# Kernel optimization log

Measured on AMD Instinct MI355X. Metric: run time of the kernel, lower is better.

The kernel has to match this reference:

```python
import jax, jax.numpy as jnp
import numpy as np

NUM_HOPS = 2
GAMMA = 0.8


def setup_inputs() -> dict:
    key = jax.random.key(0)
    ks = jax.random.split(key, 17)
    B, L, V, E, M, Mt, R = 8, 128, 50257, 768, 400, 800, 40
    W = 0.02  # init scale for learned params
    return {
        'hidden_states': jax.random.normal(ks[0], (B, L, E), jnp.float32),
        'wte': jax.random.normal(ks[1], (V, E), jnp.float32) * W,
        'rel_emb': jax.random.normal(ks[2], (R, E), jnp.float32) * W,
        'W_s': jax.random.normal(ks[3], (NUM_HOPS, E, E), jnp.float32) * W,
        'W_n': jax.random.normal(ks[4], (NUM_HOPS, E, E), jnp.float32) * W,
        'W_r': jax.random.normal(ks[5], (NUM_HOPS, E, E), jnp.float32) * W,
        'W_triple': jax.random.normal(ks[6], (E, 3 * E), jnp.float32) * W,
        'gate_w': jax.random.normal(ks[7], (E,), jnp.float32) * W,
        'gate_b': jnp.zeros((), jnp.float32),
        'concept_ids': jax.random.randint(ks[8], (B, M), 0, V),
        'relation_ids': jax.random.randint(ks[9], (B, Mt), 0, R),
        'head_idx': jax.random.randint(ks[10], (B, Mt), 0, M),
        'tail_idx': jax.random.randint(ks[11], (B, Mt), 0, M),
        'triple_labels': jax.random.randint(ks[12], (B, Mt), 0, 2),
        'distances': jax.random.randint(ks[13], (B, M), 0, 3),
        'vocab_map': jax.random.randint(ks[14], (V,), 0, M),
        'map_mask': jax.random.randint(ks[15], (V,), 0, 2),
    }


def _triple_encoder(wte, rel_emb, W_s, W_n, W_r, concept_ids, relation_ids, head_idx, tail_idx):
    concept_repr = wte[concept_ids]      # B,M,E
    rel_repr = rel_emb[relation_ids]     # B,Mt,E

    def gcn(cr, rr, h, t):               # per-batch CompGCN, faithful to torch loop
        M = cr.shape[0]
        ch, rh = cr, rr
        for l in range(NUM_HOPS):
            upd = jnp.zeros_like(cr)
            upd = upd.at[t].add(cr[h] - rr)   # scatter_add(o) + scatter_add(-rel)
            upd = upd.at[h].add(cr[t] - rr)
            cnt = jnp.zeros((M,), cr.dtype).at[t].add(1.0).at[h].add(1.0)
            upd = cr @ W_s[l].T + (upd @ W_n[l].T) / jnp.clip(cnt, 1.0, None)[:, None]
            ch = jax.nn.relu(upd)
            rh = rr @ W_r[l].T
        return ch, rh

    node, relh = jax.vmap(gcn)(concept_repr, rel_repr, head_idx, tail_idx)
    E = node.shape[-1]
    hi = jnp.broadcast_to(head_idx[:, :, None], head_idx.shape + (E,))
    ti = jnp.broadcast_to(tail_idx[:, :, None], tail_idx.shape + (E,))
    hrep = jnp.take_along_axis(node, hi, axis=1)
    trep = jnp.take_along_axis(node, ti, axis=1)
    return jnp.concatenate([hrep, relh, trep], axis=-1)  # B,Mt,3E


def _multi_hop(triple_prob, distances, head, tail):
    B, L, Mt = triple_prob.shape
    M = distances.shape[1]
    dt = triple_prob.dtype
    init_mask = jnp.broadcast_to((distances == 0).astype(dt)[:, None, :], (B, L, M))
    decay = (0.8 ** distances.astype(dt))[:, None, :]
    head_b = jnp.broadcast_to(head[:, None, :], (B, L, Mt))

    def scatter_mean(vals, t):  # vals: L,Mt  t: Mt -> L,M
        s = jnp.zeros((L, M), vals.dtype).at[:, t].add(vals)
        c = jnp.zeros((M,), vals.dtype).at[t].add(1.0)
        return s / jnp.clip(c, 1.0, None)

    node_score = init_mask
    total = init_mask * (-100000.0)
    for _ in range(NUM_HOPS):
        ths = jnp.take_along_axis(node_score, head_b, axis=2)  # B,L,Mt
        upd = ths * GAMMA + triple_prob
        node_score = jax.vmap(scatter_mean)(upd, tail)          # B,L,M
        total = total + node_score * decay
    return total


def reference(hidden_states, wte, rel_emb, W_s, W_n, W_r, W_triple, gate_w, gate_b,
              concept_ids, relation_ids, head_idx, tail_idx, triple_labels,
              distances, vocab_map, map_mask):
    triple_repr = _triple_encoder(wte, rel_emb, W_s, W_n, W_r,
                                  concept_ids, relation_ids, head_idx, tail_idx)
    lm_probs = jax.nn.softmax(hidden_states @ wte.T, axis=-1)            # B,L,V
    tl = triple_repr @ W_triple.T                                        # B,Mt,E
    triple_prob = jax.nn.sigmoid(jnp.einsum('ble,bme->blm', hidden_states, tl))
    triple_prob = triple_prob * (triple_labels != -1)[:, None, :].astype(triple_prob.dtype)
    scores = _multi_hop(triple_prob, distances, head_idx, tail_idx)      # B,L,M
    concept_probs = jax.nn.softmax(scores, axis=-1)
    cpv = concept_probs[:, :, vocab_map]                                 # gather into vocab: B,L,V
    cpv = cpv * (map_mask != 0)[None, None, :].astype(cpv.dtype)
    gate = jax.nn.sigmoid(hidden_states @ gate_w + gate_b)[..., None]    # B,L,1
    probs = gate * cpv + (1.0 - gate) * lm_probs
    return probs
```

## Files before the change

kernel.cpp:

```cpp
#include <hip/hip_runtime.h>
#include <stdint.h>

#define HB 8
#define HL 128
#define HV 50257
#define HE 768
#define HM 400
#define HMT 800
#define HBL (HB*HL)
#define NTILES 393
#define ELD 50272

typedef __attribute__((ext_vector_type(4))) float f32x4;
typedef __attribute__((ext_vector_type(8))) short bf16x8;
typedef unsigned short u16;

struct u16x4 { u16 x, y, z, w; };

__device__ __forceinline__ u16 f2bf(float x){
  union { float f; uint32_t u; } v; v.f = x;
  uint32_t r = v.u + 0x7fffu + ((v.u >> 16) & 1u);
  return (u16)(r >> 16);
}
__device__ __forceinline__ float bf2f(u16 b){
  union { uint32_t u; float f; } v; v.u = ((uint32_t)b) << 16;
  return v.f;
}
__device__ __forceinline__ void glds(const u16* g, const u16* l){
  __builtin_amdgcn_global_load_lds(
      (const __attribute__((address_space(1))) void*)g,
      (__attribute__((address_space(3))) void*)l, 16, 0, 0);
}

__global__ __launch_bounds__(256) void prep_k(const float* __restrict__ hs,
    const float* __restrict__ rel, const float* __restrict__ Wr1src,
    const float* __restrict__ Wtsrc, const float* __restrict__ Ws1,
    const float* __restrict__ Wn1, const int* __restrict__ vmap,
    const int* __restrict__ mmask, const float* __restrict__ wte,
    u16* __restrict__ hid_b, u16* __restrict__ rel_b,
    u16* __restrict__ wr1, u16* __restrict__ wt_b, u16* __restrict__ wcat,
    int* __restrict__ vmm, u16* __restrict__ wte_b){
  const int b = blockIdx.x, t = threadIdx.x;
  if (b >= 5456) {
    long i = (long)(b-5456)*256 + t;
    if (i < (long)HV*HE/4) {
      float4 x = ((const float4*)wte)[i];
      u16x4 y; y.x=f2bf(x.x); y.y=f2bf(x.y); y.z=f2bf(x.z); y.w=f2bf(x.w);
      ((u16x4*)wte_b)[i] = y;
    }
    return;
  }
  if (b < 768) {
    int i = b*256 + t;
    float4 x = ((const float4*)hs)[i];
    u16x4 y; y.x=f2bf(x.x); y.y=f2bf(x.y); y.z=f2bf(x.z); y.w=f2bf(x.w);
    ((u16x4*)hid_b)[i] = y;
  } else if (b < 798) {
    int i = (b-768)*256 + t;
    float4 x = ((const float4*)rel)[i];
    u16x4 y; y.x=f2bf(x.x); y.y=f2bf(x.y); y.z=f2bf(x.z); y.w=f2bf(x.w);
    ((u16x4*)rel_b)[i] = y;
  } else if (b < 1374) {
    int i = (b-798)*256 + t;
    float4 x = ((const float4*)Wr1src)[i];
    u16x4 y; y.x=f2bf(x.x); y.y=f2bf(x.y); y.z=f2bf(x.z); y.w=f2bf(x.w);
    ((u16x4*)wr1)[i] = y;
  } else if (b < 3102) {
    int i = (b-1374)*256 + t;
    float4 x = ((const float4*)Wtsrc)[i];
    u16x4 y; y.x=f2bf(x.x); y.y=f2bf(x.y); y.z=f2bf(x.z); y.w=f2bf(x.w);
    ((u16x4*)wt_b)[i] = y;
  } else if (b < 5406) {
    int i = (b-3102)*256 + t;
    int e = i / HE, k = i - e*HE;
    wcat[(long)e*(2*HE) + k]      = f2bf(Ws1[i]);
    wcat[(long)e*(2*HE) + HE + k] = f2bf(Wn1[i]);
  } else {
    int base = (b-5406)*1024 + t*4;
    #pragma unroll
    for (int i = 0; i < 4; ++i) {
      int c = base + i;
      if (c < HV) vmm[c] = mmask[c] ? vmap[c] : -1;
    }
  }
}

__global__ __launch_bounds__(256) void gcn_scatter_k(const float* __restrict__ wte,
    const float* __restrict__ rel, const int* __restrict__ cids,
    const int* __restrict__ rids, const int* __restrict__ head,
    const int* __restrict__ tail, u16* __restrict__ An){
  const int ch = blockIdx.x % 48;
  const int b  = blockIdx.x / 48;
  const int e0 = ch * 16;
  __shared__ float cw[HM][17];
  __shared__ float upd[HM][17];
  __shared__ float relc[40][17];
  __shared__ float cnt[HM];
  const int tid = threadIdx.x;

  for (int idx = tid; idx < HM*16; idx += 256) {
    int m = idx >> 4, e = idx & 15;
    cw[m][e] = wte[(long)cids[b*HM+m]*HE + e0 + e];
    upd[m][e] = 0.f;
  }
  for (int idx = tid; idx < 40*16; idx += 256) {
    int r = idx >> 4, e = idx & 15;
    relc[r][e] = rel[r*HE + e0 + e];
  }
  for (int m = tid; m < HM; m += 256) cnt[m] = 0.f;
  __syncthreads();

  for (int j = tid; j < HMT; j += 256) {
    int h = head[b*HMT+j], t = tail[b*HMT+j], r = rids[b*HMT+j];
    atomicAdd(&cnt[t], 1.f);
    atomicAdd(&cnt[h], 1.f);
    #pragma unroll
    for (int e = 0; e < 16; ++e) {
      float rv = relc[r][e];
      atomicAdd(&upd[t][e], cw[h][e] - rv);
      atomicAdd(&upd[h][e], cw[t][e] - rv);
    }
  }
  __syncthreads();

  for (int idx = tid; idx < HM*16; idx += 256) {
    int m = idx >> 4, e = idx & 15;
    float ic = 1.f / fmaxf(cnt[m], 1.f);
    u16* dst = An + ((long)b*HM + m) * (2*HE);
    dst[e0 + e]      = f2bf(cw[m][e]);
    dst[HE + e0 + e] = f2bf(upd[m][e] * ic);
  }
}

template<int ACT, int OUTBF16, int BIG, int DBUF>
__device__ __forceinline__ void gemm_core(
    const u16* __restrict__ Ab, const u16* __restrict__ Bb,
    void* __restrict__ Cout, float* __restrict__ rowpart,
    int Mdim, int Ndim, int Kdim, int lda, int ldb, int ldc,
    int mtile, int ntile, u16* AsmB, u16* BsmB)
{
  const int m0 = mtile * 128;
  const int n0 = ntile * 128;
  const int tid = threadIdx.x;
  const int lane = tid & 63;
  const int wid = tid >> 6;
  const int wr = wid >> 1, wc = wid & 1;
  const int srw = lane >> 3;
  const int sl  = lane & 7;

  f32x4 acc[4][4] = {};

  auto stage = [&](int buf, int k0) {
    u16* As = AsmB + buf*8192;
    u16* Bs = BsmB + buf*8192;
    #pragma unroll
    for (int i = 0; i < 4; ++i) {
      const int c = i*4 + wid;
      const int row = c*8 + srw;
      const int koff = k0 + ((sl ^ srw) * 8);
      int ra = m0 + row; if (ra > Mdim-1) ra = Mdim-1;
      glds(Ab + (long)ra * lda + koff, &As[c*512]);
      int rn = n0 + row; if (rn > Ndim-1) rn = Ndim-1;
      glds(Bb + (long)rn * ldb + koff, &Bs[c*512]);
    }
  };
  auto compute = [&](int buf) {
    const u16* As = AsmB + buf*8192;
    const u16* Bs = BsmB + buf*8192;
    #pragma unroll
    for (int kk = 0; kk < 2; ++kk) {
      bf16x8 af[4], bfr[4];
      #pragma unroll
      for (int mi = 0; mi < 4; ++mi) {
        const int R = wr*64 + mi*16 + (lane & 15);
        af[mi] = *(const bf16x8*)&As[R*64 + (((kk*4 + (lane>>4)) ^ (R & 7)) * 8)];
      }
      #pragma unroll
      for (int ni = 0; ni < 4; ++ni) {
        const int R = wc*64 + ni*16 + (lane & 15);
        bfr[ni] = *(const bf16x8*)&Bs[R*64 + (((kk*4 + (lane>>4)) ^ (R & 7)) * 8)];
      }
      #pragma unroll
      for (int mi = 0; mi < 4; ++mi)
        #pragma unroll
        for (int ni = 0; ni < 4; ++ni)
          acc[mi][ni] = __builtin_amdgcn_mfma_f32_16x16x32_bf16(af[mi], bfr[ni], acc[mi][ni], 0, 0, 0);
    }
  };

  const int NT = Kdim >> 6;
  if (DBUF) {
    stage(0, 0);
    __syncthreads();
    int cur = 0;
    for (int t = 0; t < NT; ++t) {
      if (t + 1 < NT) stage(cur ^ 1, (t + 1) << 6);
      compute(cur);
      __syncthreads();
      cur ^= 1;
    }
  } else {
    for (int t = 0; t < NT; ++t) {
      stage(0, t << 6);
      __syncthreads();
      compute(0);
      __syncthreads();
    }
  }

  const int cr0 = m0 + wr*64 + ((lane >> 4) * 4);
  const int cc0 = n0 + wc*64 + (lane & 15);

  if (BIG) {
    float* rs = (float*)AsmB;
    #pragma unroll
    for (int mi = 0; mi < 4; ++mi) {
      #pragma unroll
      for (int r = 0; r < 4; ++r) {
        const int rowi = cr0 + mi*16 + r;
        float s = 0.f;
        #pragma unroll
        for (int ni = 0; ni < 4; ++ni) {
          const int col = cc0 + ni*16;
          if (col < Ndim) {
            float e = __expf(acc[mi][ni][r]);
            if (OUTBF16) ((u16*)Cout)[(long)rowi*ELD + col] = f2bf(e);
            else        ((float*)Cout)[(long)rowi*HV + col] = e;
            s += e;
          }
        }
        s += __shfl_xor(s, 8); s += __shfl_xor(s, 4);
        s += __shfl_xor(s, 2); s += __shfl_xor(s, 1);
        if ((lane & 15) == 0)
          rs[wc*128 + wr*64 + mi*16 + ((lane >> 4) << 2) + r] = s;
      }
    }
    __syncthreads();
    if (tid < 128)
      rowpart[(long)(m0 + tid) * NTILES + ntile] = rs[tid] + rs[128 + tid];
    return;
  }

  #pragma unroll
  for (int mi = 0; mi < 4; ++mi) {
    #pragma unroll
    for (int ni = 0; ni < 4; ++ni) {
      const int col = cc0 + ni*16;
      if (col < Ndim) {
        #pragma unroll
        for (int r = 0; r < 4; ++r) {
          const int rowi = cr0 + mi*16 + r;
          if (rowi < Mdim) {
            float v = acc[mi][ni][r];
            if (ACT == 1) v = fmaxf(v, 0.f);
            if (OUTBF16) ((u16*)Cout)[(long)rowi*ldc + col] = f2bf(v);
            else        ((float*)Cout)[(long)rowi*ldc + col] = v;
          }
        }
      }
    }
  }
}

template<int ACT, int OUTBF16, int BIG>
__global__ __launch_bounds__(256) void gemm_bt(
    const u16* __restrict__ A, const u16* __restrict__ Bm,
    void* __restrict__ Cout, float* __restrict__ rowpart,
    int Mdim, int Ndim, int Kdim, int lda, int ldb, int ldc,
    long Abs, long Bbs, long Cbs)
{
  __shared__ alignas(16) u16 Asm[(BIG ? 1 : 2)*8192];
  __shared__ alignas(16) u16 Bsm[(BIG ? 1 : 2)*8192];
  int mtile, ntile, bz;
  if (BIG) {
    const int wg = (blockIdx.x & 7) * NTILES + (blockIdx.x >> 3);
    mtile = wg & 7; ntile = wg >> 3; bz = 0;
  } else {
    mtile = blockIdx.x; ntile = blockIdx.y; bz = blockIdx.z;
  }
  const u16* Ab = A + (long)bz * Abs;
  const u16* Bb = Bm + (long)bz * Bbs;
  void* Cb = OUTBF16 ? (void*)((u16*)Cout + (long)bz * Cbs)
                     : (void*)((float*)Cout + (long)bz * Cbs);
  gemm_core<ACT,OUTBF16,BIG,(BIG?0:1)>(Ab, Bb, Cb, rowpart, Mdim, Ndim, Kdim,
                                       lda, ldb, ldc, mtile, ntile, Asm, Bsm);
}

template<int PHASE>
__global__ __launch_bounds__(256) void gemm_multi(
    const u16* __restrict__ anode, const u16* __restrict__ wcat,
    u16* __restrict__ nodeb, const u16* __restrict__ rel_b,
    const u16* __restrict__ wr1, u16* __restrict__ relWr,
    const u16* __restrict__ wt_b, u16* __restrict__ P13)
{
  __shared__ alignas(16) u16 Asm[2*8192];
  __shared__ alignas(16) u16 Bsm[2*8192];
  const int mtile = blockIdx.x, ntile = blockIdx.y, z = blockIdx.z;
  if (PHASE == 0) {
    if (z < 8) {
      gemm_core<1,1,0,1>(anode + (long)z*HM*2*HE, wcat, nodeb + (long)z*HM*HE,
          nullptr, HM, HE, 2*HE, 2*HE, 2*HE, HE, mtile, ntile, Asm, Bsm);
    } else {
      if (mtile) return;
      gemm_core<0,1,0,1>(rel_b, wr1, relWr, nullptr,
          40, HE, HE, HE, HE, HE, 0, ntile, Asm, Bsm);
    }
  } else {
    if (z < 8) {
      if (mtile) return;
      gemm_core<0,1,0,1>(relWr, wt_b + HE, P13 + (long)z*840*HE + (long)800*HE,
          nullptr, 40, HE, HE, HE, 3*HE, HE, 0, ntile, Asm, Bsm);
    } else if (z < 16) {
      gemm_core<0,1,0,1>(nodeb + (long)(z-8)*HM*HE, wt_b,
          P13 + (long)(z-8)*840*HE, nullptr,
          HM, HE, HE, HE, 3*HE, HE, mtile, ntile, Asm, Bsm);
    } else {
      gemm_core<0,1,0,1>(nodeb + (long)(z-16)*HM*HE, wt_b + 2*HE,
          P13 + (long)(z-16)*840*HE + (long)HM*HE, nullptr,
          HM, HE, HE, HE, 3*HE, HE, mtile, ntile, Asm, Bsm);
    }
  }
}

__global__ __launch_bounds__(256) void multihop_k(const float* __restrict__ scores,
    const float* __restrict__ hs, const float* __restrict__ gw,
    const float* __restrict__ gb,
    const int* __restrict__ head, const int* __restrict__ tail,
    const int* __restrict__ rids, const int* __restrict__ labels,
    const int* __restrict__ dist, float* __restrict__ gatev,
    float* __restrict__ cprob){
  const int bl = blockIdx.x;
  const int b = bl >> 7;
  const int tid = threadIdx.x;
  const int lane = tid & 63, wid = tid >> 6;
  __shared__ float srow[840];
  __shared__ float tp[HMT];
  __shared__ float ns[HM], sacc[HM], tot[HM], invc[HM], dec[HM];
  __shared__ float red[16];
  __shared__ float gred[4];
  const int* hb = head + b*HMT;
  const int* tb = tail + b*HMT;
  const int* rb = rids + b*HMT;
  const int* lb = labels + b*HMT;
  const float* sr = scores + (long)bl * 840;

  float gs = 0.f;
  for (int e = tid; e < HE; e += 256) gs += hs[(long)bl*HE + e] * gw[e];
  for (int o = 32; o; o >>= 1) gs += __shfl_down(gs, o);
  if (lane == 0) gred[wid] = gs;

  for (int i = tid; i < 840; i += 256) srow[i] = sr[i];
  for (int m = tid; m < HM; m += 256) {
    int d = dist[b*HM + m];
    float im = (d == 0) ? 1.f : 0.f;
    ns[m] = im; tot[m] = im * -100000.f;
    dec[m] = (d == 0) ? 1.f : ((d == 1) ? 0.8f : 0.64f);
    sacc[m] = 0.f; invc[m] = 0.f;
  }
  __syncthreads();
  if (tid == 0)
    gatev[bl] = 1.f / (1.f + __expf(-(gred[0]+gred[1]+gred[2]+gred[3] + gb[0])));
  for (int j = tid; j < HMT; j += 256) {
    atomicAdd(&invc[tb[j]], 1.f);
    float x = srow[hb[j]] + srow[400 + tb[j]] + srow[800 + rb[j]];
    tp[j] = (lb[j] == -1) ? 0.f : 1.f / (1.f + __expf(-x));
  }
  __syncthreads();
  for (int m = tid; m < HM; m += 256) invc[m] = 1.f / fmaxf(invc[m], 1.f);
  __syncthreads();

  for (int hop = 0; hop < 2; ++hop) {
    for (int j = tid; j < HMT; j += 256) {
      float u = ns[hb[j]] * 0.8f + tp[j];
      atomicAdd(&sacc[tb[j]], u);
    }
    __syncthreads();
    for (int m = tid; m < HM; m += 256) {
      float v = sacc[m] * invc[m];
      ns[m] = v; tot[m] += v * dec[m]; sacc[m] = 0.f;
    }
    __syncthreads();
  }

  float lmx = -3.4e38f;
  for (int m = tid; m < HM; m += 256) lmx = fmaxf(lmx, tot[m]);
  for (int o = 32; o; o >>= 1) lmx = fmaxf(lmx, __shfl_down(lmx, o));
  if (lane == 0) red[wid] = lmx;
  __syncthreads();
  float gmx = fmaxf(fmaxf(red[0], red[1]), fmaxf(red[2], red[3]));
  float ls = 0.f;
  for (int m = tid; m < HM; m += 256) ls += __expf(tot[m] - gmx);
  for (int o = 32; o; o >>= 1) ls += __shfl_down(ls, o);
  if (lane == 0) red[8 + wid] = ls;
  __syncthreads();
  float inv = 1.f / (red[8] + red[9] + red[10] + red[11]);
  float* outrow = cprob + (long)bl * HM;
  for (int m = tid; m < HM; m += 256) outrow[m] = __expf(tot[m] - gmx) * inv;
}

template<int EXPBF>
__global__ __launch_bounds__(256) void finalize_k(const void* __restrict__ expl,
    const float* __restrict__ rowpart, const float* __restrict__ gatev,
    const float* __restrict__ cprob, const int* __restrict__ vmm,
    float* __restrict__ out){
  const int r = blockIdx.x / 13;
  const int ch = blockIdx.x - r*13;
  const int tid = threadIdx.x;
  __shared__ float red[4];
  __shared__ float cpl[HM];
  float s = 0.f;
  for (int t = tid; t < NTILES; t += 256) s += rowpart[r*NTILES + t];
  for (int o = 32; o; o >>= 1) s += __shfl_down(s, o);
  if ((tid & 63) == 0) red[tid >> 6] = s;
  const float g = gatev[r];
  for (int m = tid; m < HM; m += 256) cpl[m] = g * cprob[r*HM + m];
  __syncthreads();
  const float scale = (1.f - g) / (red[0] + red[1] + red[2] + red[3]);
  const u16* erb = (const u16*)expl + (long)r * ELD;
  const float* erf = (const float*)expl + (long)r * HV;
  float* orow = out + (long)r * HV;
  #pragma unroll
  for (int it = 0; it < 2; ++it) {
    const int c = ch*4096 + it*2048 + tid*8;
    if (c + 8 <= HV) {
      float e[8];
      if (EXPBF) {
        bf16x8 v = *(const bf16x8*)&erb[c];
        #pragma unroll
        for (int i = 0; i < 8; ++i) e[i] = bf2f((u16)v[i]);
      } else {
        float4 a = *(const float4*)&erf[c];
        float4 b2 = *(const float4*)&erf[c+4];
        e[0]=a.x; e[1]=a.y; e[2]=a.z; e[3]=a.w;
        e[4]=b2.x; e[5]=b2.y; e[6]=b2.z; e[7]=b2.w;
      }
      int4 v0 = *(const int4*)&vmm[c];
      int4 v1 = *(const int4*)&vmm[c+4];
      const int ix[8] = {v0.x, v0.y, v0.z, v0.w, v1.x, v1.y, v1.z, v1.w};
      float o8[8];
      #pragma unroll
      for (int i = 0; i < 8; ++i)
        o8[i] = (ix[i] >= 0 ? cpl[ix[i]] : 0.f) + scale * e[i];
      *(float4*)&orow[c]   = make_float4(o8[0], o8[1], o8[2], o8[3]);
      *(float4*)&orow[c+4] = make_float4(o8[4], o8[5], o8[6], o8[7]);
    } else if (c < HV) {
      for (int i = 0; i < 8 && c + i < HV; ++i) {
        float e = EXPBF ? bf2f(((const u16*)expl)[(long)r*ELD + c + i]) : erf[c+i];
        int ix = vmm[c+i];
        orow[c+i] = (ix >= 0 ? cpl[ix] : 0.f) + scale * e;
      }
    }
  }
}

extern "C" void kernel_launch(void* const* d_in, const int* in_sizes, int n_in,
                              void* d_out, int out_size, void* d_ws, size_t ws_size,
                              hipStream_t stream)
{
  const float* hs   = (const float*)d_in[0];
  const float* wte  = (const float*)d_in[1];
  const float* rel  = (const float*)d_in[2];
  const float* Ws   = (const float*)d_in[3];
  const float* Wn   = (const float*)d_in[4];
  const float* Wr   = (const float*)d_in[5];
  const float* Wt   = (const float*)d_in[6];
  const float* gw   = (const float*)d_in[7];
  const float* gb   = (const float*)d_in[8];
  const int* cids   = (const int*)d_in[9];
  const int* rids   = (const int*)d_in[10];
  const int* head   = (const int*)d_in[11];
  const int* tail   = (const int*)d_in[12];
  const int* labels = (const int*)d_in[13];
  const int* dist   = (const int*)d_in[14];
  const int* vmap   = (const int*)d_in[15];
  const int* mmask  = (const int*)d_in[16];
  float* out = (float*)d_out;

  char* ws = (char*)d_ws;
  size_t o = 0;
  auto alloc = [&](size_t bytes) -> char* {
    char* p = ws + o; o = (o + bytes + 255) & ~(size_t)255; return p;
  };
  u16* wte_b     = (u16*)alloc((size_t)HV*HE*2);
  u16* hid_b     = (u16*)alloc((size_t)HBL*HE*2);
  float* cprob   = (float*)alloc((size_t)HBL*HM*4);
  float* rowpart = (float*)alloc((size_t)HBL*NTILES*4);
  float* gatev   = (float*)alloc(HBL*4);
  int* vmm       = (int*)alloc((size_t)HV*4);

  const bool bigws = ws_size >= (size_t)196*1024*1024;
  u16* expl = (u16*)(ws + o);
  u16* wcat  = (u16*)alloc((size_t)HE*2*HE*2);
  u16* wr1   = (u16*)alloc((size_t)HE*HE*2);
  u16* wt_b  = (u16*)alloc((size_t)HE*3*HE*2);
  u16* rel_b = (u16*)alloc((size_t)40*HE*2);
  u16* anode = (u16*)alloc((size_t)HB*HM*2*HE*2);
  u16* nodeb = (u16*)alloc((size_t)HB*HM*HE*2);
  u16* relWr = (u16*)alloc((size_t)40*HE*2);
  float* scores = (float*)alloc((size_t)HB*HL*840*4);
  u16* P13   = (u16*)alloc((size_t)HB*840*HE*2);
  (void)in_sizes; (void)n_in; (void)out_size;

  prep_k<<<5456 + 37693, 256, 0, stream>>>(hs, rel, Wr + (size_t)HE*HE, Wt,
      Ws + (size_t)HE*HE, Wn + (size_t)HE*HE, vmap, mmask, wte,
      hid_b, rel_b, wr1, wt_b, wcat, vmm, wte_b);

  gcn_scatter_k<<<HB*48, 256, 0, stream>>>(wte, rel, cids, rids, head, tail, anode);

  gemm_multi<0><<<dim3(4,6,9), 256, 0, stream>>>(anode, wcat, nodeb,
      rel_b, wr1, relWr, wt_b, P13);
  gemm_multi<1><<<dim3(4,6,24), 256, 0, stream>>>(anode, wcat, nodeb,
      rel_b, wr1, relWr, wt_b, P13);
  gemm_bt<0,0,0><<<dim3(1,7,8), 256, 0, stream>>>(hid_b, P13, scores,
      nullptr, HL, 840, HE, HE, HE, 840, (long)HL*HE, (long)840*HE, (long)HL*840);

  multihop_k<<<HBL, 256, 0, stream>>>(scores, hs, gw, gb, head, tail, rids,
      labels, dist, gatev, cprob);

  if (bigws) {
    gemm_bt<0,1,1><<<3144, 256, 0, stream>>>(hid_b, wte_b, expl, rowpart,
        HBL, HV, HE, HE, HE, ELD, 0, 0, 0);
    finalize_k<1><<<HBL*13, 256, 0, stream>>>(expl, rowpart, gatev, cprob,
        vmm, out);
  } else {
    gemm_bt<0,0,1><<<3144, 256, 0, stream>>>(hid_b, wte_b, out, rowpart,
        HBL, HV, HE, HE, HE, HV, 0, 0, 0);
    finalize_k<0><<<HBL*13, 256, 0, stream>>>(out, rowpart, gatev, cprob,
        vmm, out);
  }
}
```

Measured before the change: 449.2 us.

## Reassociate triple scoring through hidden·W_triple and fuse multihop into vocab GEMM

The triple-score path is reassociated: instead of projecting node and relation representations through W_triple and then multiplying by hidden states, hidden states are first multiplied by a transposed W_triple (hw = hid·Wt), and then scored against node and relation embeddings. This removes the per-batch P13 intermediate and merges the small GEMMs into two flat-grid launches. The multihop softmax kernel is folded into the large vocab GEMM launch as extra blocks sharing a union of shared memory, which cuts launches and lets that work overlap with the GEMM. The cost is a strided, uncoalesced transpose of W_triple in prep and larger shared memory per block for the fused kernel.

```diff
diff --git a/kernel.cpp b/kernel.cpp
--- a/kernel.cpp
+++ b/kernel.cpp
@@ -34,11 +34,11 @@
 
 __global__ __launch_bounds__(256) void prep_k(const float* __restrict__ hs,
     const float* __restrict__ rel, const float* __restrict__ Wr1src,
-    const float* __restrict__ Wtsrc, const float* __restrict__ Ws1,
+    const float* __restrict__ Wt, const float* __restrict__ Ws1,
     const float* __restrict__ Wn1, const int* __restrict__ vmap,
     const int* __restrict__ mmask, const float* __restrict__ wte,
     u16* __restrict__ hid_b, u16* __restrict__ rel_b,
-    u16* __restrict__ wr1, u16* __restrict__ wt_b, u16* __restrict__ wcat,
+    u16* __restrict__ wr1, u16* __restrict__ wtT, u16* __restrict__ wcat,
     int* __restrict__ vmm, u16* __restrict__ wte_b){
   const int b = blockIdx.x, t = threadIdx.x;
   if (b >= 5456) {
@@ -66,10 +66,14 @@
     u16x4 y; y.x=f2bf(x.x); y.y=f2bf(x.y); y.z=f2bf(x.z); y.w=f2bf(x.w);
     ((u16x4*)wr1)[i] = y;
   } else if (b < 3102) {
-    int i = (b-1374)*256 + t;
-    float4 x = ((const float4*)Wtsrc)[i];
-    u16x4 y; y.x=f2bf(x.x); y.y=f2bf(x.y); y.z=f2bf(x.z); y.w=f2bf(x.w);
-    ((u16x4*)wt_b)[i] = y;
+    int g = (b-1374)*256 + t;
+    int f = g / 192, r = g - f*192, e0 = r*4;
+    u16x4 y;
+    y.x = f2bf(Wt[(long)(e0+0)*2304 + f]);
+    y.y = f2bf(Wt[(long)(e0+1)*2304 + f]);
+    y.z = f2bf(Wt[(long)(e0+2)*2304 + f]);
+    y.w = f2bf(Wt[(long)(e0+3)*2304 + f]);
+    *(u16x4*)&wtT[(long)f*HE + e0] = y;
   } else if (b < 5406) {
     int i = (b-3102)*256 + t;
     int e = i / HE, k = i - e*HE;
@@ -262,82 +266,70 @@
   }
 }
 
-template<int ACT, int OUTBF16, int BIG>
-__global__ __launch_bounds__(256) void gemm_bt(
-    const u16* __restrict__ A, const u16* __restrict__ Bm,
-    void* __restrict__ Cout, float* __restrict__ rowpart,
-    int Mdim, int Ndim, int Kdim, int lda, int ldb, int ldc,
-    long Abs, long Bbs, long Cbs)
-{
-  __shared__ alignas(16) u16 Asm[(BIG ? 1 : 2)*8192];
-  __shared__ alignas(16) u16 Bsm[(BIG ? 1 : 2)*8192];
-  int mtile, ntile, bz;
-  if (BIG) {
-    const int wg = (blockIdx.x & 7) * NTILES + (blockIdx.x >> 3);
-    mtile = wg & 7; ntile = wg >> 3; bz = 0;
-  } else {
-    mtile = blockIdx.x; ntile = blockIdx.y; bz = blockIdx.z;
-  }
-  const u16* Ab = A + (long)bz * Abs;
-  const u16* Bb = Bm + (long)bz * Bbs;
-  void* Cb = OUTBF16 ? (void*)((u16*)Cout + (long)bz * Cbs)
-                     : (void*)((float*)Cout + (long)bz * Cbs);
-  gemm_core<ACT,OUTBF16,BIG,(BIG?0:1)>(Ab, Bb, Cb, rowpart, Mdim, Ndim, Kdim,
-                                       lda, ldb, ldc, mtile, ntile, Asm, Bsm);
-}
-
-template<int PHASE>
-__global__ __launch_bounds__(256) void gemm_multi(
+__global__ __launch_bounds__(256) void gemm_multi0(
     const u16* __restrict__ anode, const u16* __restrict__ wcat,
     u16* __restrict__ nodeb, const u16* __restrict__ rel_b,
     const u16* __restrict__ wr1, u16* __restrict__ relWr,
-    const u16* __restrict__ wt_b, u16* __restrict__ P13)
+    const u16* __restrict__ hid_b, const u16* __restrict__ wtT,
+    u16* __restrict__ hw)
 {
   __shared__ alignas(16) u16 Asm[2*8192];
   __shared__ alignas(16) u16 Bsm[2*8192];
-  const int mtile = blockIdx.x, ntile = blockIdx.y, z = blockIdx.z;
-  if (PHASE == 0) {
-    if (z < 8) {
-      gemm_core<1,1,0,1>(anode + (long)z*HM*2*HE, wcat, nodeb + (long)z*HM*HE,
-          nullptr, HM, HE, 2*HE, 2*HE, 2*HE, HE, mtile, ntile, Asm, Bsm);
-    } else {
-      if (mtile) return;
-      gemm_core<0,1,0,1>(rel_b, wr1, relWr, nullptr,
-          40, HE, HE, HE, HE, HE, 0, ntile, Asm, Bsm);
-    }
+  const int q = blockIdx.x;
+  if (q < 192) {
+    const int z = q / 24, r = q - z*24;
+    gemm_core<1,1,0,1>(anode + (long)z*HM*2*HE, wcat, nodeb + (long)z*HM*HE,
+        nullptr, HM, HE, 2*HE, 2*HE, 2*HE, HE, r & 3, r >> 2, Asm, Bsm);
+  } else if (q < 198) {
+    gemm_core<0,1,0,1>(rel_b, wr1, relWr, nullptr,
+        40, HE, HE, HE, HE, HE, 0, q - 192, Asm, Bsm);
   } else {
-    if (z < 8) {
-      if (mtile) return;
-      gemm_core<0,1,0,1>(relWr, wt_b + HE, P13 + (long)z*840*HE + (long)800*HE,
-          nullptr, 40, HE, HE, HE, 3*HE, HE, 0, ntile, Asm, Bsm);
-    } else if (z < 16) {
-      gemm_core<0,1,0,1>(nodeb + (long)(z-8)*HM*HE, wt_b,
-          P13 + (long)(z-8)*840*HE, nullptr,
-          HM, HE, HE, HE, 3*HE, HE, mtile, ntile, Asm, Bsm);
-    } else {
-      gemm_core<0,1,0,1>(nodeb + (long)(z-16)*HM*HE, wt_b + 2*HE,
-          P13 + (long)(z-16)*840*HE + (long)HM*HE, nullptr,
-          HM, HE, HE, HE, 3*HE, HE, mtile, ntile, Asm, Bsm);
-    }
-  }
-}
-
-__global__ __launch_bounds__(256) void multihop_k(const float* __restrict__ scores,
-    const float* __restrict__ hs, const float* __restrict__ gw,
-    const float* __restrict__ gb,
+    const int u = q - 198;
+    gemm_core<0,1,0,1>(hid_b, wtT, hw, nullptr,
+        HBL, 3*HE, HE, HE, HE, 3*HE, u & 7, u >> 3, Asm, Bsm);
+  }
+}
+
+__global__ __launch_bounds__(256) void gemm_multi1(
+    const u16* __restrict__ hw, const u16* __restrict__ nodeb,
+    const u16* __restrict__ relWr, float* __restrict__ scores)
+{
+  __shared__ alignas(16) u16 Asm[2*8192];
+  __shared__ alignas(16) u16 Bsm[2*8192];
+  const int q = blockIdx.x;
+  if (q < 32) {
+    const int z = q >> 2;
+    gemm_core<0,0,0,1>(hw + (long)z*HL*(3*HE), nodeb + (long)z*HM*HE,
+        scores + (long)z*HL*840, nullptr,
+        HL, HM, HE, 3*HE, HE, 840, 0, q & 3, Asm, Bsm);
+  } else if (q < 64) {
+    const int z = (q - 32) >> 2;
+    gemm_core<0,0,0,1>(hw + (long)z*HL*(3*HE) + 2*HE, nodeb + (long)z*HM*HE,
+        scores + (long)z*HL*840 + HM, nullptr,
+        HL, HM, HE, 3*HE, HE, 840, 0, (q - 32) & 3, Asm, Bsm);
+  } else {
+    gemm_core<0,0,0,1>(hw + HE, relWr, scores + 2*HM, nullptr,
+        HBL, 40, HE, 3*HE, HE, 840, q - 64, 0, Asm, Bsm);
+  }
+}
+
+union SmemU {
+  struct { u16 A[8192]; u16 B[8192]; } g;
+  struct { float srow[840]; float tp[HMT]; float ns[HM]; float sacc[HM];
+           float tot[HM]; float invc[HM]; float dec[HM];
+           float red[16]; float gred[4]; } m;
+};
+
+__device__ __forceinline__ void multihop_dev(SmemU& sm,
+    const float* __restrict__ scores, const float* __restrict__ hs,
+    const float* __restrict__ gw, const float* __restrict__ gb,
     const int* __restrict__ head, const int* __restrict__ tail,
     const int* __restrict__ rids, const int* __restrict__ labels,
     const int* __restrict__ dist, float* __restrict__ gatev,
-    float* __restrict__ cprob){
-  const int bl = blockIdx.x;
+    float* __restrict__ cprob, int bl){
   const int b = bl >> 7;
   const int tid = threadIdx.x;
   const int lane = tid & 63, wid = tid >> 6;
-  __shared__ float srow[840];
-  __shared__ float tp[HMT];
-  __shared__ float ns[HM], sacc[HM], tot[HM], invc[HM], dec[HM];
-  __shared__ float red[16];
-  __shared__ float gred[4];
   const int* hb = head + b*HMT;
   const int* tb = tail + b*HMT;
   const int* rb = rids + b*HMT;
@@ -347,55 +339,79 @@
   float gs = 0.f;
   for (int e = tid; e < HE; e += 256) gs += hs[(long)bl*HE + e] * gw[e];
   for (int o = 32; o; o >>= 1) gs += __shfl_down(gs, o);
-  if (lane == 0) gred[wid] = gs;
-
-  for (int i = tid; i < 840; i += 256) srow[i] = sr[i];
+  if (lane == 0) sm.m.gred[wid] = gs;
+
+  for (int i = tid; i < 840; i += 256) sm.m.srow[i] = sr[i];
   for (int m = tid; m < HM; m += 256) {
     int d = dist[b*HM + m];
     float im = (d == 0) ? 1.f : 0.f;
-    ns[m] = im; tot[m] = im * -100000.f;
-    dec[m] = (d == 0) ? 1.f : ((d == 1) ? 0.8f : 0.64f);
-    sacc[m] = 0.f; invc[m] = 0.f;
+    sm.m.ns[m] = im; sm.m.tot[m] = im * -100000.f;
+    sm.m.dec[m] = (d == 0) ? 1.f : ((d == 1) ? 0.8f : 0.64f);
+    sm.m.sacc[m] = 0.f; sm.m.invc[m] = 0.f;
   }
   __syncthreads();
   if (tid == 0)
-    gatev[bl] = 1.f / (1.f + __expf(-(gred[0]+gred[1]+gred[2]+gred[3] + gb[0])));
+    gatev[bl] = 1.f / (1.f + __expf(-(sm.m.gred[0]+sm.m.gred[1]+sm.m.gred[2]+sm.m.gred[3] + gb[0])));
   for (int j = tid; j < HMT; j += 256) {
-    atomicAdd(&invc[tb[j]], 1.f);
-    float x = srow[hb[j]] + srow[400 + tb[j]] + srow[800 + rb[j]];
-    tp[j] = (lb[j] == -1) ? 0.f : 1.f / (1.f + __expf(-x));
-  }
-  __syncthreads();
-  for (int m = tid; m < HM; m += 256) invc[m] = 1.f / fmaxf(invc[m], 1.f);
+    atomicAdd(&sm.m.invc[tb[j]], 1.f);
+    float x = sm.m.srow[hb[j]] + sm.m.srow[HM + tb[j]] + sm.m.srow[2*HM + rb[j]];
+    sm.m.tp[j] = (lb[j] == -1) ? 0.f : 1.f / (1.f + __expf(-x));
+  }
+  __syncthreads();
+  for (int m = tid; m < HM; m += 256) sm.m.invc[m] = 1.f / fmaxf(sm.m.invc[m], 1.f);
   __syncthreads();
 
   for (int hop = 0; hop < 2; ++hop) {
     for (int j = tid; j < HMT; j += 256) {
-      float u = ns[hb[j]] * 0.8f + tp[j];
-      atomicAdd(&sacc[tb[j]], u);
+      float u = sm.m.ns[hb[j]] * 0.8f + sm.m.tp[j];
+      atomicAdd(&sm.m.sacc[tb[j]], u);
     }
     __syncthreads();
     for (int m = tid; m < HM; m += 256) {
-      float v = sacc[m] * invc[m];
-      ns[m] = v; tot[m] += v * dec[m]; sacc[m] = 0.f;
+      float v = sm.m.sacc[m] * sm.m.invc[m];
+      sm.m.ns[m] = v; sm.m.tot[m] += v * sm.m.dec[m]; sm.m.sacc[m] = 0.f;
     }
     __syncthreads();
   }
 
   float lmx = -3.4e38f;
-  for (int m = tid; m < HM; m += 256) lmx = fmaxf(lmx, tot[m]);
+  for (int m = tid; m < HM; m += 256) lmx = fmaxf(lmx, sm.m.tot[m]);
   for (int o = 32; o; o >>= 1) lmx = fmaxf(lmx, __shfl_down(lmx, o));
-  if (lane == 0) red[wid] = lmx;
-  __syncthreads();
-  float gmx = fmaxf(fmaxf(red[0], red[1]), fmaxf(red[2], red[3]));
+  if (lane == 0) sm.m.red[wid] = lmx;
+  __syncthreads();
+  float gmx = fmaxf(fmaxf(sm.m.red[0], sm.m.red[1]), fmaxf(sm.m.red[2], sm.m.red[3]));
   float ls = 0.f;
-  for (int m = tid; m < HM; m += 256) ls += __expf(tot[m] - gmx);
+  for (int m = tid; m < HM; m += 256) ls += __expf(sm.m.tot[m] - gmx);
   for (int o = 32; o; o >>= 1) ls += __shfl_down(ls, o);
-  if (lane == 0) red[8 + wid] = ls;
-  __syncthreads();
-  float inv = 1.f / (red[8] + red[9] + red[10] + red[11]);
+  if (lane == 0) sm.m.red[8 + wid] = ls;
+  __syncthreads();
+  float inv = 1.f / (sm.m.red[8] + sm.m.red[9] + sm.m.red[10] + sm.m.red[11]);
   float* outrow = cprob + (long)bl * HM;
-  for (int m = tid; m < HM; m += 256) outrow[m] = __expf(tot[m] - gmx) * inv;
+  for (int m = tid; m < HM; m += 256) outrow[m] = __expf(sm.m.tot[m] - gmx) * inv;
+}
+
+template<int EXPBF>
+__global__ __launch_bounds__(256) void big_fused(
+    const u16* __restrict__ hid_b, const u16* __restrict__ wte_b,
+    void* __restrict__ expl, float* __restrict__ rowpart,
+    const float* __restrict__ scores, const float* __restrict__ hs,
+    const float* __restrict__ gw, const float* __restrict__ gb,
+    const int* __restrict__ head, const int* __restrict__ tail,
+    const int* __restrict__ rids, const int* __restrict__ labels,
+    const int* __restrict__ dist, float* __restrict__ gatev,
+    float* __restrict__ cprob)
+{
+  __shared__ SmemU sm;
+  if (blockIdx.x < HBL) {
+    multihop_dev(sm, scores, hs, gw, gb, head, tail, rids, labels, dist,
+                 gatev, cprob, blockIdx.x);
+    return;
+  }
+  const int bid = blockIdx.x - HBL;
+  const int wg = (bid & 7) * NTILES + (bid >> 3);
+  gemm_core<0,EXPBF,1,0>(hid_b, wte_b, expl, rowpart,
+      HBL, HV, HE, HE, HE, (EXPBF ? ELD : HV), wg & 7, wg >> 3,
+      sm.g.A, sm.g.B);
 }
 
 template<int EXPBF>
@@ -487,44 +503,38 @@
   float* rowpart = (float*)alloc((size_t)HBL*NTILES*4);
   float* gatev   = (float*)alloc(HBL*4);
   int* vmm       = (int*)alloc((size_t)HV*4);
+  float* scores  = (float*)alloc((size_t)HBL*840*4);
 
   const bool bigws = ws_size >= (size_t)196*1024*1024;
   u16* expl = (u16*)(ws + o);
   u16* wcat  = (u16*)alloc((size_t)HE*2*HE*2);
   u16* wr1   = (u16*)alloc((size_t)HE*HE*2);
-  u16* wt_b  = (u16*)alloc((size_t)HE*3*HE*2);
+  u16* wtT   = (u16*)alloc((size_t)3*HE*HE*2);
   u16* rel_b = (u16*)alloc((size_t)40*HE*2);
   u16* anode = (u16*)alloc((size_t)HB*HM*2*HE*2);
   u16* nodeb = (u16*)alloc((size_t)HB*HM*HE*2);
   u16* relWr = (u16*)alloc((size_t)40*HE*2);
-  float* scores = (float*)alloc((size_t)HB*HL*840*4);
-  u16* P13   = (u16*)alloc((size_t)HB*840*HE*2);
+  u16* hw    = (u16*)alloc((size_t)HBL*3*HE*2);
   (void)in_sizes; (void)n_in; (void)out_size;
 
   prep_k<<<5456 + 37693, 256, 0, stream>>>(hs, rel, Wr + (size_t)HE*HE, Wt,
       Ws + (size_t)HE*HE, Wn + (size_t)HE*HE, vmap, mmask, wte,
-      hid_b, rel_b, wr1, wt_b, wcat, vmm, wte_b);
+      hid_b, rel_b, wr1, wtT, wcat, vmm, wte_b);
 
   gcn_scatter_k<<<HB*48, 256, 0, stream>>>(wte, rel, cids, rids, head, tail, anode);
 
-  gemm_multi<0><<<dim3(4,6,9), 256, 0, stream>>>(anode, wcat, nodeb,
-      rel_b, wr1, relWr, wt_b, P13);
-  gemm_multi<1><<<dim3(4,6,24), 256, 0, stream>>>(anode, wcat, nodeb,
-      rel_b, wr1, relWr, wt_b, P13);
-  gemm_bt<0,0,0><<<dim3(1,7,8), 256, 0, stream>>>(hid_b, P13, scores,
-      nullptr, HL, 840, HE, HE, HE, 840, (long)HL*HE, (long)840*HE, (long)HL*840);
-
-  multihop_k<<<HBL, 256, 0, stream>>>(scores, hs, gw, gb, head, tail, rids,
-      labels, dist, gatev, cprob);
+  gemm_multi0<<<342, 256, 0, stream>>>(anode, wcat, nodeb, rel_b, wr1, relWr,
+      hid_b, wtT, hw);
+  gemm_multi1<<<72, 256, 0, stream>>>(hw, nodeb, relWr, scores);
 
   if (bigws) {
-    gemm_bt<0,1,1><<<3144, 256, 0, stream>>>(hid_b, wte_b, expl, rowpart,
-        HBL, HV, HE, HE, HE, ELD, 0, 0, 0);
+    big_fused<1><<<HBL + 3144, 256, 0, stream>>>(hid_b, wte_b, expl, rowpart,
+        scores, hs, gw, gb, head, tail, rids, labels, dist, gatev, cprob);
     finalize_k<1><<<HBL*13, 256, 0, stream>>>(expl, rowpart, gatev, cprob,
         vmm, out);
   } else {
-    gemm_bt<0,0,1><<<3144, 256, 0, stream>>>(hid_b, wte_b, out, rowpart,
-        HBL, HV, HE, HE, HE, HV, 0, 0, 0);
+    big_fused<0><<<HBL + 3144, 256, 0, stream>>>(hid_b, wte_b, out, rowpart,
+        scores, hs, gw, gb, head, tail, rids, labels, dist, gatev, cprob);
     finalize_k<0><<<HBL*13, 256, 0, stream>>>(out, rowpart, gatev, cprob,
         vmm, out);
   }
```

Measured after the change: 453.8 us. Within noise of the previous version (+1.0%).
